# Kernel tuning notes

Hardware: AMD Instinct MI355X
Metric: run time of the kernel (lower is better)

## Reference

```python
import jax, jax.numpy as jnp
import numpy as np

KERNEL_SIZE = 5
SIGMA = 2.0
HALF_K = KERNEL_SIZE // 2


def _gaussian_kernel():
    # torch: arange(-k//2+1, k//2+1) with python floor div -> [-2,...,2] for k=5
    ax = jnp.arange(-(KERNEL_SIZE // 2), KERNEL_SIZE // 2 + 1, dtype=jnp.float32)
    xx, yy = jnp.meshgrid(ax, ax, indexing='ij')
    k = jnp.exp(-(xx ** 2 + yy ** 2) / (2.0 * SIGMA ** 2))
    return k / k.sum()  # [5,5]


def setup_inputs() -> dict:
    key = jax.random.key(0)
    k1, k2 = jax.random.split(key)
    feature_map = jax.random.normal(k1, (512, 256, 256), dtype=jnp.float32)
    keypoints = jax.random.randint(k2, (4096, 2), 0, 256, dtype=jnp.int64)
    return {"feature_map": feature_map, "keypoints": keypoints}


def reference(feature_map, keypoints):
    C, H, W = feature_map.shape
    kern = _gaussian_kernel().astype(feature_map.dtype)  # [5,5]
    x = jnp.clip(keypoints[:, 0].astype(jnp.int32), HALF_K, W - HALF_K - 1)  # [N]
    y = jnp.clip(keypoints[:, 1].astype(jnp.int32), HALF_K, H - HALF_K - 1)  # [N]

    def pool_one(xi, yi):
        patch = jax.lax.dynamic_slice(
            feature_map, (0, yi - HALF_K, xi - HALF_K), (C, KERNEL_SIZE, KERNEL_SIZE)
        )  # [C,5,5]
        return jnp.einsum('chw,hw->c', patch, kern)  # [C]

    return jax.vmap(pool_one)(x, y)  # [N,C]
```

## Files before the change

### kernel.cpp

```cpp
#include <hip/hip_runtime.h>


#define NC  512
#define NH  256
#define NW  256
#define NKP 4096

#define NSTRIP 16
#define RING_ROWS 64

#define WS_LIST_OFF_I 8192

__global__ __launch_bounds__(256) void bucket_kernel(
    const int* __restrict__ kp, unsigned* __restrict__ ws_i, int n_kp)
{
    __shared__ int hist[NSTRIP];
    __shared__ int base[NSTRIP];
    const int t = threadIdx.x;
    const int i = blockIdx.x * 256 + t;

    if (t < NSTRIP) hist[t] = 0;
    __syncthreads();

    int q = 0, lr = 0;
    unsigned pk = 0;
    const bool valid = (i < n_kp);
    if (valid) {
        int x = kp[2 * i + 0];
        int y = kp[2 * i + 1];
        x = min(max(x, 2), NW - 3);
        y = min(max(y, 2), NH - 3);
        q  = y >> 4;
        lr = atomicAdd(&hist[q], 1);
        pk = (unsigned)i | ((unsigned)x << 12) | ((unsigned)y << 20);
    }
    __syncthreads();

    if (t < NSTRIP) base[t] = atomicAdd((int*)&ws_i[t], hist[t]);
    __syncthreads();

    if (valid)
        ws_i[WS_LIST_OFF_I + q * NKP + base[q] + lr] = pk;
}

__global__ __launch_bounds__(256) void pool_kernel(
    const float* __restrict__ fm, const unsigned* __restrict__ ws_i,
    float* __restrict__ out)
{
    __shared__ float ring[RING_ROWS * NW];

    const int c = blockIdx.x;
    const int t = threadIdx.x;
    const float* plane = fm + ((size_t)c << 16);

    const float e1 = 0.8824969025845955f;
    const float e2 = 0.6065306597126334f;
    const float s2 = 2.0f * (e1 + e2) + 1.0f;
    const float inv_s2 = 1.0f / (s2 * s2);
    const float g[5] = {e2, e1, 1.0f, e1, e2};
    float gy[5];
#pragma unroll
    for (int i = 0; i < 5; i++) gy[i] = g[i] * inv_s2;

    float4 pf[4];

    for (int s = -2; s < NSTRIP; ++s) {
        const int sp = s + 2;

        if (sp < NSTRIP) {
            const float4* src = (const float4*)(plane + (sp << 12));
#pragma unroll
            for (int j = 0; j < 4; ++j)
                pf[j] = src[t + j * 256];
        }

        if (s >= 0) {
            const int cnt = (int)ws_i[s];
            const unsigned* list = ws_i + WS_LIST_OFF_I + s * NKP;
            for (int e = t; e < cnt; e += 256) {
                const unsigned pk = list[e];
                const int n  = (int)(pk & 0xFFFu);
                const int xc = (int)((pk >> 12) & 0xFFu);
                const int yc = (int)((pk >> 20) & 0xFFu);

                const int x0 = xc - 2;
                const int r  = x0 & 3;
                const int xa = x0 - r;
                float wx[8];
#pragma unroll
                for (int i = 0; i < 8; i++)
                    wx[i] = (i >= r && i < r + 5) ? g[i - r] : 0.0f;

                float acc = 0.0f;
#pragma unroll
                for (int dy = 0; dy < 5; dy++) {
                    const int gr = yc - 2 + dy;
                    const float* rowp = &ring[((gr & (RING_ROWS - 1)) << 8) + xa];
                    float4 a = *(const float4*)rowp;
                    float4 b = *(const float4*)(rowp + 4);
                    acc += gy[dy] * (a.x * wx[0] + a.y * wx[1] + a.z * wx[2] + a.w * wx[3]
                                   + b.x * wx[4] + b.y * wx[5] + b.z * wx[6] + b.w * wx[7]);
                }
                out[(size_t)n * NC + c] = acc;
            }
        }

        __syncthreads();

        if (sp < NSTRIP) {
            float* dst = &ring[(sp & 3) << 12];
#pragma unroll
            for (int j = 0; j < 4; ++j)
                *(float4*)&dst[(t + j * 256) << 2] = pf[j];
        }

        __syncthreads();
    }
}

__global__ __launch_bounds__(256) void gpool_direct_kernel(
    const float* __restrict__ fm, const int* __restrict__ kp,
    float* __restrict__ out)
{
    const int n = blockIdx.x;
    const int t = threadIdx.x;

    int x = kp[2 * n + 0];
    int y = kp[2 * n + 1];
    x = min(max(x, 2), NW - 3);
    y = min(max(y, 2), NH - 3);

    const float e1 = 0.8824969025845955f;
    const float e2 = 0.6065306597126334f;
    const float s  = 2.0f * (e1 + e2) + 1.0f;
    const float inv_s2 = 1.0f / (s * s);
    float g[5] = {e2, e1, 1.0f, e1, e2};
    float gy[5];
#pragma unroll
    for (int i = 0; i < 5; i++) gy[i] = g[i] * inv_s2;

    const int x0 = x - 2;
    const int r  = x0 & 3;
    const int xa = x0 - r;
    float wx[8];
#pragma unroll
    for (int i = 0; i < 8; i++)
        wx[i] = (i >= r && i < r + 5) ? g[i - r] : 0.0f;

    const float* base0 = fm + ((size_t)t * NH + (y - 2)) * NW + xa;
    const float* base1 = fm + ((size_t)(t + 256) * NH + (y - 2)) * NW + xa;

    float acc0 = 0.0f, acc1 = 0.0f;
#pragma unroll
    for (int dy = 0; dy < 5; dy++) {
        const float4* p0 = (const float4*)(base0 + dy * NW);
        const float4* p1 = (const float4*)(base1 + dy * NW);
        float4 a0 = p0[0], b0 = p0[1], a1 = p1[0], b1 = p1[1];
        acc0 += gy[dy] * (a0.x * wx[0] + a0.y * wx[1] + a0.z * wx[2] + a0.w * wx[3]
                        + b0.x * wx[4] + b0.y * wx[5] + b0.z * wx[6] + b0.w * wx[7]);
        acc1 += gy[dy] * (a1.x * wx[0] + a1.y * wx[1] + a1.z * wx[2] + a1.w * wx[3]
                        + b1.x * wx[4] + b1.y * wx[5] + b1.z * wx[6] + b1.w * wx[7]);
    }

    out[(size_t)n * NC + t]       = acc0;
    out[(size_t)n * NC + t + 256] = acc1;
}

extern "C" void kernel_launch(void* const* d_in, const int* in_sizes, int n_in,
                              void* d_out, int out_size, void* d_ws, size_t ws_size,
                              hipStream_t stream)
{
    const float* fm  = (const float*)d_in[0];
    const int*   kp  = (const int*)d_in[1];
    float*       out = (float*)d_out;
    const int n_kp   = in_sizes[1] / 2;

    const size_t need = (WS_LIST_OFF_I + (size_t)NSTRIP * NKP) * sizeof(unsigned);
    if (ws_size >= need && n_kp == NKP) {
        unsigned* ws_i = (unsigned*)d_ws;

        hipMemsetAsync(d_ws, 0, NSTRIP * sizeof(unsigned), stream);

        bucket_kernel<<<(NKP + 255) / 256, 256, 0, stream>>>(kp, ws_i, n_kp);

        pool_kernel<<<NC, 256, 0, stream>>>(fm, ws_i, out);
    } else {
        gpool_direct_kernel<<<n_kp, 256, 0, stream>>>(fm, kp, out);
    }
}
```

Baseline: 227.6 us.

## Shrink pool strips to 8 rows, pad LDS ring, remap channels, single-block bucketing

```diff
diff --git a/kernel.cpp b/kernel.cpp
--- a/kernel.cpp
+++ b/kernel.cpp
@@ -6,72 +6,72 @@
 #define NW  256
 #define NKP 4096
 
-#define NSTRIP 16
-#define RING_ROWS 64
+#define NSTRIP 32
+#define RING_ROWS 32
+#define STR 260
 
 #define WS_LIST_OFF_I 8192
 
-__global__ __launch_bounds__(256) void bucket_kernel(
+__global__ __launch_bounds__(1024) void bucket_kernel(
     const int* __restrict__ kp, unsigned* __restrict__ ws_i, int n_kp)
 {
     __shared__ int hist[NSTRIP];
-    __shared__ int base[NSTRIP];
     const int t = threadIdx.x;
-    const int i = blockIdx.x * 256 + t;
-
     if (t < NSTRIP) hist[t] = 0;
     __syncthreads();
 
-    int q = 0, lr = 0;
-    unsigned pk = 0;
-    const bool valid = (i < n_kp);
-    if (valid) {
-        int x = kp[2 * i + 0];
-        int y = kp[2 * i + 1];
-        x = min(max(x, 2), NW - 3);
-        y = min(max(y, 2), NH - 3);
-        q  = y >> 4;
-        lr = atomicAdd(&hist[q], 1);
-        pk = (unsigned)i | ((unsigned)x << 12) | ((unsigned)y << 20);
+#pragma unroll
+    for (int k = 0; k < 4; ++k) {
+        const int i = t + k * 1024;
+        if (i < n_kp) {
+            int x = kp[2 * i + 0];
+            int y = kp[2 * i + 1];
+            x = min(max(x, 2), NW - 3);
+            y = min(max(y, 2), NH - 3);
+            const int q = y >> 3;
+            const int pos = atomicAdd(&hist[q], 1);
+            ws_i[WS_LIST_OFF_I + q * NKP + pos] =
+                (unsigned)i | ((unsigned)x << 12) | ((unsigned)y << 20);
+        }
     }
     __syncthreads();
-
-    if (t < NSTRIP) base[t] = atomicAdd((int*)&ws_i[t], hist[t]);
-    __syncthreads();
-
-    if (valid)
-        ws_i[WS_LIST_OFF_I + q * NKP + base[q] + lr] = pk;
+    if (t < NSTRIP) ws_i[t] = (unsigned)hist[t];
 }
 
 __global__ __launch_bounds__(256) void pool_kernel(
     const float* __restrict__ fm, const unsigned* __restrict__ ws_i,
     float* __restrict__ out)
 {
-    __shared__ float ring[RING_ROWS * NW];
+    __shared__ float ring[RING_ROWS * STR];
 
-    const int c = blockIdx.x;
+    const int b      = blockIdx.x;
+    const int x7     = b & 7;
+    const int inner  = b >> 3;
+    const int lane16 = inner & 15;
+    const int hi     = inner >> 4;
+    const int chunk  = (hi << 3) | x7;
+    const int c      = (chunk << 4) | lane16;
+
     const int t = threadIdx.x;
-    const float* plane = fm + ((size_t)c << 16);
+    const float4* src = (const float4*)(fm + ((size_t)c << 16));
 
     const float e1 = 0.8824969025845955f;
     const float e2 = 0.6065306597126334f;
-    const float s2 = 2.0f * (e1 + e2) + 1.0f;
-    const float inv_s2 = 1.0f / (s2 * s2);
+    const float sN = 2.0f * (e1 + e2) + 1.0f;
+    const float inv_s2 = 1.0f / (sN * sN);
     const float g[5] = {e2, e1, 1.0f, e1, e2};
     float gy[5];
 #pragma unroll
     for (int i = 0; i < 5; i++) gy[i] = g[i] * inv_s2;
 
-    float4 pf[4];
+    float4 pf0, pf1;
 
     for (int s = -2; s < NSTRIP; ++s) {
         const int sp = s + 2;
 
         if (sp < NSTRIP) {
-            const float4* src = (const float4*)(plane + (sp << 12));
-#pragma unroll
-            for (int j = 0; j < 4; ++j)
-                pf[j] = src[t + j * 256];
+            pf0 = src[(sp << 9) + t];
+            pf1 = src[(sp << 9) + 256 + t];
         }
 
         if (s >= 0) {
@@ -95,11 +95,11 @@
 #pragma unroll
                 for (int dy = 0; dy < 5; dy++) {
                     const int gr = yc - 2 + dy;
-                    const float* rowp = &ring[((gr & (RING_ROWS - 1)) << 8) + xa];
-                    float4 a = *(const float4*)rowp;
-                    float4 b = *(const float4*)(rowp + 4);
+                    const float* rowp = &ring[(gr & (RING_ROWS - 1)) * STR + xa];
+                    float4 a  = *(const float4*)rowp;
+                    float4 b4 = *(const float4*)(rowp + 4);
                     acc += gy[dy] * (a.x * wx[0] + a.y * wx[1] + a.z * wx[2] + a.w * wx[3]
-                                   + b.x * wx[4] + b.y * wx[5] + b.z * wx[6] + b.w * wx[7]);
+                                   + b4.x * wx[4] + b4.y * wx[5] + b4.z * wx[6] + b4.w * wx[7]);
                 }
                 out[(size_t)n * NC + c] = acc;
             }
@@ -108,10 +108,19 @@
         __syncthreads();
 
         if (sp < NSTRIP) {
-            float* dst = &ring[(sp & 3) << 12];
-#pragma unroll
-            for (int j = 0; j < 4; ++j)
-                *(float4*)&dst[(t + j * 256) << 2] = pf[j];
+            {
+                const int row  = t >> 6;
+                const int col4 = t & 63;
+                const int pr   = ((sp << 3) + row) & (RING_ROWS - 1);
+                *(float4*)&ring[pr * STR + (col4 << 2)] = pf0;
+            }
+            {
+                const int j    = t + 256;
+                const int row  = j >> 6;
+                const int col4 = j & 63;
+                const int pr   = ((sp << 3) + row) & (RING_ROWS - 1);
+                *(float4*)&ring[pr * STR + (col4 << 2)] = pf1;
+            }
         }
 
         __syncthreads();
@@ -179,10 +188,7 @@
     if (ws_size >= need && n_kp == NKP) {
         unsigned* ws_i = (unsigned*)d_ws;
 
-        hipMemsetAsync(d_ws, 0, NSTRIP * sizeof(unsigned), stream);
-
-        bucket_kernel<<<(NKP + 255) / 256, 256, 0, stream>>>(kp, ws_i, n_kp);
-
+        bucket_kernel<<<1, 1024, 0, stream>>>(kp, ws_i, n_kp);
         pool_kernel<<<NC, 256, 0, stream>>>(fm, ws_i, out);
     } else {
         gpool_direct_kernel<<<n_kp, 256, 0, stream>>>(fm, kp, out);
```

New measurement: 219.6 us. 3.5% less time.
